# Optimization experiments

Hardware: AMD Instinct MI355X
Metric: run time of the kernel (lower is better)

Reference implementation:

```python
import jax, jax.numpy as jnp
import numpy as np

N, M, D_IN, D_OUT = 4096, 16384, 256, 256


def setup_inputs() -> dict:
    key = jax.random.key(0)
    k1, k2, k3, k4 = jax.random.split(key, 4)
    query = jax.random.normal(k1, (N, D_IN), dtype=jnp.float32)
    # bandwidths bounded away from zero for numerical sanity
    std = jax.random.uniform(k2, (N,), dtype=jnp.float32, minval=0.5, maxval=1.5)
    source_db = jax.random.normal(k3, (M, D_OUT), dtype=jnp.float32)
    target_db = jax.random.normal(k4, (M, D_IN), dtype=jnp.float32)
    return {"query": query, "std": std, "source_db": source_db, "target_db": target_db}


def reference(query, std, source_db, target_db):
    # Squared L2 distances [N, M] via the GEMM expansion (avoids the NxMxD diff
    # tensor the torch code materializes; same math).
    q_sq = jnp.sum(query * query, axis=1, keepdims=True)          # [N, 1]
    t_sq = jnp.sum(target_db * target_db, axis=1)                 # [M]
    cross = query @ target_db.T                                   # [N, M]
    dist = q_sq + t_sq[None, :] - 2.0 * cross                     # [N, M]
    # Gaussian kernel logits and stable softmax over the database axis.
    x = -dist / (2.0 * std[:, None] ** 2)                         # [N, M]
    w = jax.nn.softmax(x, axis=1)                                 # [N, M]
    # Nadaraya-Watson weighted sum of source values -> [N, D_OUT].
    return w @ source_db
```

## Files before the change

kernel.cpp:

```cpp
#include <hip/hip_runtime.h>


#define N_Q 4096
#define M_DB 16384
#define D_K 256
#define NCC 17
#define BQ 256
#define BM 32
#define NCHUNK 16
#define MC (M_DB / NCHUNK)
#define NTILE (MC / BM)
#define LOG2E 1.44269504088896f
#define THR 8.0f
#define TOFF 17408
#define TILE_B 33792

typedef _Float16 f16;
typedef _Float16 f16x2v __attribute__((ext_vector_type(2)));
typedef _Float16 f16x4v __attribute__((ext_vector_type(4)));
typedef _Float16 f16x8 __attribute__((ext_vector_type(8)));
typedef float f32x4 __attribute__((ext_vector_type(4)));
typedef float f32x16 __attribute__((ext_vector_type(16)));
typedef unsigned short u16;
typedef unsigned int u32;
typedef u32 u32x4 __attribute__((ext_vector_type(4)));

typedef const __attribute__((address_space(1))) void cg_void;
typedef __attribute__((address_space(3))) void lds_void;

__device__ __forceinline__ void gload16(const void* g, void* s) {
  __builtin_amdgcn_global_load_lds((cg_void*)g, (lds_void*)s, 16, 0, 0);
}

__global__ void k_prep_q(const float* __restrict__ q, char* __restrict__ qpk) {
  int qt = blockIdx.x;
  int t = threadIdx.x;
  for (int i = 0; i < 5; i++) {
    int slot = t + 256 * i;
    if (slot >= NCC * 64) break;
    int c = slot >> 6, l = slot & 63;
    int row = qt * 32 + (l & 31);
    int k0 = c * 16 + (l >> 5) * 8;
    f16x8 o;
    for (int e = 0; e < 8; e++) {
      int k = k0 + e;
      float v = (k < D_K) ? q[(size_t)row * D_K + k] : ((k <= D_K + 1) ? 1.0f : 0.0f);
      o[e] = (f16)v;
    }
    *(f16x8*)(qpk + (size_t)qt * TOFF + slot * 16) = o;
  }
}

__global__ void k_prep_tv(const float* __restrict__ tdb, const float* __restrict__ src,
                          char* __restrict__ pkTV) {
  int ti = blockIdx.x;
  int t = threadIdx.x;
  __shared__ float tsq[32];
  {
    int r = t >> 3, seg = t & 7;
    const float* p = tdb + (size_t)(ti * 32 + r) * D_K + seg * 32;
    float s = 0.f;
    for (int j = 0; j < 32; j++) { float x = p[j]; s += x * x; }
    s += __shfl_xor(s, 1); s += __shfl_xor(s, 2); s += __shfl_xor(s, 4);
    if (seg == 0) tsq[r] = 0.5f * s;
  }
  __syncthreads();
  for (int i = 0; i < 5; i++) {
    int slot = t + 256 * i;
    if (slot >= NCC * 64) break;
    int c = slot >> 6, l = slot & 63;
    int row = l & 31;
    int k0 = c * 16 + (l >> 5) * 8;
    float ts = tsq[row];
    f16 th = (f16)(-ts);
    f16x8 o;
    for (int e = 0; e < 8; e++) {
      int k = k0 + e;
      f16 h;
      if (k < D_K)            h = (f16)tdb[(size_t)(ti * 32 + row) * D_K + k];
      else if (k == D_K)      h = th;
      else if (k == D_K + 1)  h = (f16)(-ts - (float)th);
      else                    h = (f16)0.f;
      o[e] = h;
    }
    *(f16x8*)(pkTV + (size_t)ti * TILE_B + slot * 16) = o;
  }
  for (int i = 0; i < 4; i++) {
    int slot = t + 256 * i;
    int sub = slot >> 6, l = slot & 63;
    int kh = sub >> 3, db = sub & 7;
    int m = ti * 32 + kh * 16 + (l >> 5) * 8;
    int d = db * 32 + (l & 31);
    f16x8 o;
    for (int e = 0; e < 8; e++) o[e] = (f16)src[(size_t)(m + e) * D_K + d];
    *(f16x8*)(pkTV + (size_t)ti * TILE_B + TOFF + slot * 16) = o;
  }
}

__launch_bounds__(512, 2)
__global__ void k_main(const char* __restrict__ qpk, const char* __restrict__ pkTV,
                       const float* __restrict__ stdv,
                       u16* __restrict__ pO, float* __restrict__ pm, float* __restrict__ pl)
{
  __shared__ __align__(16) char su[4 * TILE_B];

  const int bid = blockIdx.x, chunk = bid & 15, qblk = bid >> 4;
  const int tid = threadIdx.x;
  const int w = tid >> 6, l = tid & 63;
  const int lq = l & 31, hi = l >> 5;

  const int qrow = qblk * BQ + w * 32 + lq;
  const float sd = stdv[qrow];
  const float is2l = LOG2E / (sd * sd);

  f16x8 qf[NCC];
  {
    const char* qb = qpk + (size_t)(qblk * 8 + w) * TOFF + l * 16;
#pragma unroll
    for (int c = 0; c < NCC; c++) qf[c] = *(const f16x8*)(qb + c * 1024);
  }

  f32x16 acc[8];
#pragma unroll
  for (int db = 0; db < 8; db++)
#pragma unroll
    for (int j = 0; j < 16; j++) acc[db][j] = 0.f;
  float mrun = -3.0e38f, lrun = 0.f;

  const size_t tbase = (size_t)chunk * NTILE;

  auto stage = [&](int t, int buf) {
    const char* g = pkTV + (tbase + t) * TILE_B;
    char* sb = &su[0] + buf * TILE_B;
#pragma unroll
    for (int i = 0; i < 4; i++)
      gload16(g + i * 8192 + tid * 16, sb + i * 8192 + w * 1024);
    if (l < 8) gload16(g + 32768 + w * 128 + l * 16, sb + 32768 + w * 128);
  };

  auto body = [&](int t) {
    const int cur = t & 3;
    f32x16 sA, sB;
#pragma unroll
    for (int j = 0; j < 16; j++) { sA[j] = 0.f; sB[j] = 0.f; }
    const char* tb = &su[0] + cur * TILE_B + l * 16;
    __builtin_amdgcn_s_setprio(1);
#pragma unroll
    for (int c = 0; c < NCC - 1; c += 2) {
      sA = __builtin_amdgcn_mfma_f32_32x32x16_f16(*(const f16x8*)(tb + c * 1024), qf[c], sA, 0, 0, 0);
      sB = __builtin_amdgcn_mfma_f32_32x32x16_f16(*(const f16x8*)(tb + (c + 1) * 1024), qf[c + 1], sB, 0, 0, 0);
    }
    sA = __builtin_amdgcn_mfma_f32_32x32x16_f16(*(const f16x8*)(tb + 16 * 1024), qf[16], sA, 0, 0, 0);
    __builtin_amdgcn_s_setprio(0);

    float l2[16];
#pragma unroll
    for (int j = 0; j < 16; j++) l2[j] = (sA[j] + sB[j]) * is2l;

    float a0 = fmaxf(l2[0], l2[1]),  a1 = fmaxf(l2[2], l2[3]);
    float a2 = fmaxf(l2[4], l2[5]),  a3 = fmaxf(l2[6], l2[7]);
    float a4 = fmaxf(l2[8], l2[9]),  a5 = fmaxf(l2[10], l2[11]);
    float a6 = fmaxf(l2[12], l2[13]), a7 = fmaxf(l2[14], l2[15]);
    float px = fmaxf(fmaxf(fmaxf(a0, a1), fmaxf(a2, a3)),
                     fmaxf(fmaxf(a4, a5), fmaxf(a6, a7)));
    px = fmaxf(px, __shfl_xor(px, 32));

    if (__any(px > mrun + THR)) {
      const float mnew = fmaxf(mrun, px);
      const float cl = exp2f(mrun - mnew);
      mrun = mnew; lrun *= cl;
#pragma unroll
      for (int db = 0; db < 8; db++)
#pragma unroll
        for (int j = 0; j < 16; j++) acc[db][j] *= cl;
    }
    float pr[16];
#pragma unroll
    for (int j = 0; j < 16; j++) pr[j] = exp2f(l2[j] - mrun);
    float s0 = (pr[0] + pr[1]) + (pr[2] + pr[3]);
    float s1 = (pr[4] + pr[5]) + (pr[6] + pr[7]);
    float s2 = (pr[8] + pr[9]) + (pr[10] + pr[11]);
    float s3 = (pr[12] + pr[13]) + (pr[14] + pr[15]);
    float ls = (s0 + s1) + (s2 + s3);
    ls += __shfl_xor(ls, 32);
    lrun += ls;

    u32 pk[8], xk[8];
#pragma unroll
    for (int j = 0; j < 8; j++) {
      f16x2v v; v[0] = (f16)pr[2 * j]; v[1] = (f16)pr[2 * j + 1];
      pk[j] = __builtin_bit_cast(u32, v);
    }
#pragma unroll
    for (int j = 0; j < 8; j++) xk[j] = (u32)__shfl_xor((int)pk[j], 32);
    const bool h = (hi != 0);
    u32x4 w0 = { h ? xk[2] : pk[0], h ? xk[3] : pk[1],
                 h ? pk[2] : xk[0], h ? pk[3] : xk[1] };
    u32x4 w1 = { h ? xk[6] : pk[4], h ? xk[7] : pk[5],
                 h ? pk[6] : xk[4], h ? pk[7] : xk[5] };
    f16x8 B0 = __builtin_bit_cast(f16x8, w0);
    f16x8 B1 = __builtin_bit_cast(f16x8, w1);

    const char* vb = &su[0] + cur * TILE_B + TOFF + l * 16;
    __builtin_amdgcn_s_setprio(1);
#pragma unroll
    for (int db = 0; db < 8; db++)
      acc[db] = __builtin_amdgcn_mfma_f32_32x32x16_f16(*(const f16x8*)(vb + db * 1024), B0, acc[db], 0, 0, 0);
#pragma unroll
    for (int db = 0; db < 8; db++)
      acc[db] = __builtin_amdgcn_mfma_f32_32x32x16_f16(*(const f16x8*)(vb + 8192 + db * 1024), B1, acc[db], 0, 0, 0);
    __builtin_amdgcn_s_setprio(0);
  };

  stage(0, 0);
  stage(1, 1);
  asm volatile("s_waitcnt vmcnt(0)" ::: "memory");
  __builtin_amdgcn_s_barrier();

  for (int s = 0; s < NTILE; s += 2) {
    if (s + 2 < NTILE) stage(s + 2, (s + 2) & 3);
    if (s + 3 < NTILE) stage(s + 3, (s + 3) & 3);
    body(s);
    body(s + 1);
    if (s + 2 < NTILE) {
      asm volatile("s_waitcnt vmcnt(0)" ::: "memory");
      __builtin_amdgcn_s_barrier();
    }
  }

  const float inv = 1.0f / lrun;
#pragma unroll
  for (int db = 0; db < 8; db++) {
#pragma unroll
    for (int g = 0; g < 4; g++) {
      f16x4v o4;
#pragma unroll
      for (int r4 = 0; r4 < 4; r4++) o4[r4] = (f16)(acc[db][g * 4 + r4] * inv);
      const int d = db * 32 + g * 8 + hi * 4;
      *(f16x4v*)(pO + ((size_t)chunk * N_Q + qrow) * D_K + d) = o4;
    }
  }
  if (hi == 0) {
    pm[(size_t)chunk * N_Q + qrow] = mrun;
    pl[(size_t)chunk * N_Q + qrow] = lrun;
  }
}

__global__ void k_combine(const u16* __restrict__ pO, const float* __restrict__ pm,
                          const float* __restrict__ pl, float* __restrict__ out)
{
  const int t = threadIdx.x;
  const int n = blockIdx.x * 8 + (t >> 5);
  const int j = t & 31;
  float M = -3.0e38f;
#pragma unroll
  for (int c = 0; c < NCHUNK; c++) M = fmaxf(M, pm[(size_t)c * N_Q + n]);
  float den = 0.f;
  float o[8];
#pragma unroll
  for (int e = 0; e < 8; e++) o[e] = 0.f;
#pragma unroll
  for (int c = 0; c < NCHUNK; c++) {
    const float wl = exp2f(pm[(size_t)c * N_Q + n] - M) * pl[(size_t)c * N_Q + n];
    den += wl;
    const f16x8 v = *(const f16x8*)(pO + ((size_t)c * N_Q + n) * D_K + j * 8);
#pragma unroll
    for (int e = 0; e < 8; e++) o[e] += wl * (float)v[e];
  }
  const float inv = 1.0f / den;
  f32x4 w0, w1;
#pragma unroll
  for (int e = 0; e < 4; e++) { w0[e] = o[e] * inv; w1[e] = o[4 + e] * inv; }
  float* dst = out + (size_t)n * D_K + j * 8;
  *(f32x4*)dst = w0;
  *(f32x4*)(dst + 4) = w1;
}

extern "C" void kernel_launch(void* const* d_in, const int* in_sizes, int n_in,
                              void* d_out, int out_size, void* d_ws, size_t ws_size,
                              hipStream_t stream)
{
  const float* q    = (const float*)d_in[0];
  const float* stdv = (const float*)d_in[1];
  const float* src  = (const float*)d_in[2];
  const float* tdb  = (const float*)d_in[3];
  float* out = (float*)d_out;

  char* wsp = (char*)d_ws;
  char* qpk = wsp;        wsp += (size_t)(N_Q / 32) * TOFF;
  char* pkTV = wsp;       wsp += (size_t)(M_DB / 32) * TILE_B;
  u16* pO = (u16*)wsp;    wsp += (size_t)NCHUNK * N_Q * D_K * 2;
  float* pm = (float*)wsp; wsp += (size_t)NCHUNK * N_Q * 4;
  float* pl = (float*)wsp; wsp += (size_t)NCHUNK * N_Q * 4;

  hipLaunchKernelGGL(k_prep_q,  dim3(N_Q / 32), dim3(256), 0, stream, q, qpk);
  hipLaunchKernelGGL(k_prep_tv, dim3(M_DB / 32), dim3(256), 0, stream, tdb, src, pkTV);
  hipLaunchKernelGGL(k_main,    dim3((N_Q / BQ) * NCHUNK), dim3(512), 0, stream,
                     qpk, pkTV, stdv, pO, pm, pl);
  hipLaunchKernelGGL(k_combine, dim3(N_Q / 8), dim3(256), 0, stream, pO, pm, pl, out);
}
```

Measured before the change: 117.2 us.

## Software-pipeline QK of next tile with PV of current tile, triple-buffer LDS

Restructures the main loop so the score MFMAs for tile t+1 are interleaved with the PV MFMAs for tile t. The softmax work of one tile can then overlap matrix-core work instead of stalling between phases. LDS buffering drops from four tiles to three, with one-tile-ahead prefetch and a barrier every tile instead of every two. The extra barriers and the live sA/sB registers across iterations may add sync overhead and register pressure.

Result: slower. 124.1 us (+5.9%).

```diff
diff --git a/kernel.cpp b/kernel.cpp
--- a/kernel.cpp
+++ b/kernel.cpp
@@ -102,7 +102,7 @@
                        const float* __restrict__ stdv,
                        u16* __restrict__ pO, float* __restrict__ pm, float* __restrict__ pl)
 {
-  __shared__ __align__(16) char su[4 * TILE_B];
+  __shared__ __align__(16) char su[3 * TILE_B];
 
   const int bid = blockIdx.x, chunk = bid & 15, qblk = bid >> 4;
   const int tid = threadIdx.x;
@@ -138,12 +138,15 @@
     if (l < 8) gload16(g + 32768 + w * 128 + l * 16, sb + 32768 + w * 128);
   };
 
-  auto body = [&](int t) {
-    const int cur = t & 3;
-    f32x16 sA, sB;
+  f32x16 sA, sB;
+
+  stage(0, 0); stage(1, 1);
+  asm volatile("s_waitcnt vmcnt(0)" ::: "memory");
+  __builtin_amdgcn_s_barrier();
+  {
 #pragma unroll
     for (int j = 0; j < 16; j++) { sA[j] = 0.f; sB[j] = 0.f; }
-    const char* tb = &su[0] + cur * TILE_B + l * 16;
+    const char* tb = &su[0] + l * 16;
     __builtin_amdgcn_s_setprio(1);
 #pragma unroll
     for (int c = 0; c < NCC - 1; c += 2) {
@@ -152,11 +155,15 @@
     }
     sA = __builtin_amdgcn_mfma_f32_32x32x16_f16(*(const f16x8*)(tb + 16 * 1024), qf[16], sA, 0, 0, 0);
     __builtin_amdgcn_s_setprio(0);
+  }
+
+  for (int t = 0; t < NTILE; ++t) {
+    const int cur = t % 3, nxt = (t + 1) % 3;
+    if (t + 2 < NTILE) stage(t + 2, (t + 2) % 3);
 
     float l2[16];
 #pragma unroll
     for (int j = 0; j < 16; j++) l2[j] = (sA[j] + sB[j]) * is2l;
-
     float a0 = fmaxf(l2[0], l2[1]),  a1 = fmaxf(l2[2], l2[3]);
     float a2 = fmaxf(l2[4], l2[5]),  a3 = fmaxf(l2[6], l2[7]);
     float a4 = fmaxf(l2[8], l2[9]),  a5 = fmaxf(l2[10], l2[11]);
@@ -203,26 +210,29 @@
 
     const char* vb = &su[0] + cur * TILE_B + TOFF + l * 16;
     __builtin_amdgcn_s_setprio(1);
-#pragma unroll
-    for (int db = 0; db < 8; db++)
-      acc[db] = __builtin_amdgcn_mfma_f32_32x32x16_f16(*(const f16x8*)(vb + db * 1024), B0, acc[db], 0, 0, 0);
-#pragma unroll
-    for (int db = 0; db < 8; db++)
-      acc[db] = __builtin_amdgcn_mfma_f32_32x32x16_f16(*(const f16x8*)(vb + 8192 + db * 1024), B1, acc[db], 0, 0, 0);
+    if (t + 1 < NTILE) {
+      const char* tb = &su[0] + nxt * TILE_B + l * 16;
+#pragma unroll
+      for (int j = 0; j < 16; j++) { sA[j] = 0.f; sB[j] = 0.f; }
+#pragma unroll
+      for (int i = 0; i < 8; i++) {
+        sA = __builtin_amdgcn_mfma_f32_32x32x16_f16(*(const f16x8*)(tb + (2 * i) * 1024), qf[2 * i], sA, 0, 0, 0);
+        acc[i] = __builtin_amdgcn_mfma_f32_32x32x16_f16(*(const f16x8*)(vb + i * 1024), B0, acc[i], 0, 0, 0);
+        sB = __builtin_amdgcn_mfma_f32_32x32x16_f16(*(const f16x8*)(tb + (2 * i + 1) * 1024), qf[2 * i + 1], sB, 0, 0, 0);
+        acc[i] = __builtin_amdgcn_mfma_f32_32x32x16_f16(*(const f16x8*)(vb + 8192 + i * 1024), B1, acc[i], 0, 0, 0);
+      }
+      sA = __builtin_amdgcn_mfma_f32_32x32x16_f16(*(const f16x8*)(tb + 16 * 1024), qf[16], sA, 0, 0, 0);
+    } else {
+#pragma unroll
+      for (int db = 0; db < 8; db++)
+        acc[db] = __builtin_amdgcn_mfma_f32_32x32x16_f16(*(const f16x8*)(vb + db * 1024), B0, acc[db], 0, 0, 0);
+#pragma unroll
+      for (int db = 0; db < 8; db++)
+        acc[db] = __builtin_amdgcn_mfma_f32_32x32x16_f16(*(const f16x8*)(vb + 8192 + db * 1024), B1, acc[db], 0, 0, 0);
+    }
     __builtin_amdgcn_s_setprio(0);
-  };
-
-  stage(0, 0);
-  stage(1, 1);
-  asm volatile("s_waitcnt vmcnt(0)" ::: "memory");
-  __builtin_amdgcn_s_barrier();
-
-  for (int s = 0; s < NTILE; s += 2) {
-    if (s + 2 < NTILE) stage(s + 2, (s + 2) & 3);
-    if (s + 3 < NTILE) stage(s + 3, (s + 3) & 3);
-    body(s);
-    body(s + 1);
-    if (s + 2 < NTILE) {
+
+    if (t < NTILE - 1) {
       asm volatile("s_waitcnt vmcnt(0)" ::: "memory");
       __builtin_amdgcn_s_barrier();
     }
```
